# Kernel optimization log

Measured on AMD Instinct MI355X. Metric: run time of the kernel, lower is better.

## Reference

```python
import jax, jax.numpy as jnp
import numpy as np

NF, NA, NC = 100000, 400, 30   # flight, airport, carrier node counts
N = NF + NA + NC               # total nodes after type concatenation
D = 256                        # hidden_channels
B = 3                          # num_bases
R = 4                          # num_relations
E = 250000                     # edges per relation


def setup_inputs() -> dict:
    key = jax.random.key(0)
    ks = jax.random.split(key, 32)
    inp = {
        'x_flight': jax.random.normal(ks[0], (NF, 32), jnp.float32),
        'x_airport': jax.random.normal(ks[1], (NA, 16), jnp.float32),
        'x_carrier': jax.random.normal(ks[2], (NC, 8), jnp.float32),
        # per-type encoders (Linear stored as [in, out])
        'W_f': jax.random.normal(ks[3], (32, D), jnp.float32) * 0.05,
        'b_f': jnp.zeros((D,), jnp.float32),
        'W_a': jax.random.normal(ks[4], (16, D), jnp.float32) * 0.05,
        'b_a': jnp.zeros((D,), jnp.float32),
        'W_c': jax.random.normal(ks[5], (8, D), jnp.float32) * 0.05,
        'b_c': jnp.zeros((D,), jnp.float32),
        # RGCNConv layer 0: basis decomposition W_r = sum_b comp[r,b] * basis[b]
        'basis0': jax.random.normal(ks[6], (B, D, D), jnp.float32) * 0.02,
        'comp0': jax.random.normal(ks[7], (R, B), jnp.float32) * 0.5,
        'root0': jax.random.normal(ks[8], (D, D), jnp.float32) * 0.02,
        'bias0': jnp.zeros((D,), jnp.float32),
        # RGCNConv layer 1
        'basis1': jax.random.normal(ks[9], (B, D, D), jnp.float32) * 0.02,
        'comp1': jax.random.normal(ks[10], (R, B), jnp.float32) * 0.5,
        'root1': jax.random.normal(ks[11], (D, D), jnp.float32) * 0.02,
        'bias1': jnp.zeros((D,), jnp.float32),
        # readout Linear(D -> 1)
        'W_out': jax.random.normal(ks[12], (D, 1), jnp.float32) * 0.05,
        'b_out': jnp.zeros((1,), jnp.float32),
        # per-relation edge lists (local indices within src/dst node type)
        'src0': jax.random.randint(ks[13], (E,), 0, NF),
        'dst0': jax.random.randint(ks[14], (E,), 0, NA),
        'src1': jax.random.randint(ks[15], (E,), 0, NA),
        'dst1': jax.random.randint(ks[16], (E,), 0, NF),
        'src2': jax.random.randint(ks[17], (E,), 0, NF),
        'dst2': jax.random.randint(ks[18], (E,), 0, NC),
        'src3': jax.random.randint(ks[19], (E,), 0, NC),
        'dst3': jax.random.randint(ks[20], (E,), 0, NF),
    }
    return inp


def _rgcn_conv(x, basis, comp, root, bias, edges):
    """PyG RGCNConv with basis decomposition, mean aggregation per relation."""
    W = jnp.einsum('rb,bio->rio', comp, basis)  # [R, D, D]
    out = x @ root + bias                        # root/self transform
    for r, (src, dst) in enumerate(edges):       # R=4 fixed relations
        msg = x[src] @ W[r]                                        # [E, D]
        agg = jax.ops.segment_sum(msg, dst, num_segments=N)        # [N, D]
        deg = jax.ops.segment_sum(jnp.ones((dst.shape[0],), x.dtype), dst,
                                  num_segments=N)
        out = out + agg / jnp.maximum(deg, 1.0)[:, None]           # mean aggr
    return out


def reference(x_flight, x_airport, x_carrier,
              W_f, b_f, W_a, b_a, W_c, b_c,
              basis0, comp0, root0, bias0,
              basis1, comp1, root1, bias1,
              W_out, b_out,
              src0, dst0, src1, dst1, src2, dst2, src3, dst3):
    # per-type encoders + ReLU, then concat into homogeneous node tensor
    hf = jax.nn.relu(x_flight @ W_f + b_f)
    ha = jax.nn.relu(x_airport @ W_a + b_a)
    hc = jax.nn.relu(x_carrier @ W_c + b_c)
    x = jnp.concatenate([hf, ha, hc], axis=0)  # offsets: flight=0, airport=NF, carrier=NF+NA
    edges = [
        (src0, dst0 + NF),        # flight -> airport
        (src1 + NF, dst1),        # airport -> flight
        (src2, dst2 + NF + NA),   # flight -> carrier
        (src3 + NF + NA, dst3),   # carrier -> flight
    ]
    x = jax.nn.relu(_rgcn_conv(x, basis0, comp0, root0, bias0, edges))
    x = jax.nn.relu(_rgcn_conv(x, basis1, comp1, root1, bias1, edges))
    # dropout is identity in eval mode
    return (x[:NF] @ W_out + b_out).squeeze(-1)  # [NF]
```

## Files before the change

### kernel.cpp

```cpp
#include <hip/hip_runtime.h>
#include <hip/hip_bf16.h>
#include <cstdint>
#include <cstddef>

constexpr int NF = 100000;
constexpr int NA = 400;
constexpr int NC = 30;
constexpr int NN = NF + NA + NC;
constexpr int D  = 256;
constexpr int DD = D * D;
constexpr int E  = 250000;
constexpr int NSL = 128;
constexpr int FBLK = (NF + 127) / 128;

typedef __attribute__((ext_vector_type(8))) short bf16x8;
typedef __attribute__((ext_vector_type(4))) float f32x4;
typedef __attribute__((ext_vector_type(8))) ushort u16x8;

__device__ inline ushort f2bf(float f) {
    __hip_bfloat16 h = __float2bfloat16(f);
    return __builtin_bit_cast(ushort, h);
}
__device__ inline float bf2f(ushort u) {
    __hip_bfloat16 h = __builtin_bit_cast(__hip_bfloat16, u);
    return __bfloat162float(h);
}

__device__ inline void gload_lds16(const ushort* g, ushort* l) {
    __builtin_amdgcn_global_load_lds(
        (const __attribute__((address_space(1))) void*)g,
        (__attribute__((address_space(3))) void*)l, 16, 0, 0);
}

__global__ __launch_bounds__(512) void encode_mfma_kernel(
    const float* __restrict__ xf,
    const ushort* __restrict__ WtH8, const ushort* __restrict__ WtL8,
    const float* __restrict__ bfl,
    const float* __restrict__ xa, const float* __restrict__ Wa, const float* __restrict__ ba,
    const float* __restrict__ xc, const float* __restrict__ Wc, const float* __restrict__ bc,
    ushort* __restrict__ hH)
{
    const int t = threadIdx.x;
    const int b = blockIdx.x;
    if (b >= FBLK) {
        int c = t & 255;
        int i0 = t >> 8;
        int base = (b - FBLK) * 8;
        for (int i = i0; i < 8; i += 2) {
            int row = base + i;
            if (row >= NA + NC) break;
            float acc;
            if (row < NA) {
                const float* xr = xa + (size_t)row * 16;
                acc = ba[c];
                #pragma unroll
                for (int k = 0; k < 16; ++k) acc += xr[k] * Wa[k * D + c];
            } else {
                const float* xr = xc + (size_t)(row - NA) * 8;
                acc = bc[c];
                #pragma unroll
                for (int k = 0; k < 8; ++k) acc += xr[k] * Wc[k * D + c];
            }
            hH[(size_t)(NF + row) * D + c] = f2bf(fmaxf(acc, 0.f));
        }
        return;
    }
    constexpr int AOFF = 0, WHOFF = 4096, WLOFF = 12288;
    __shared__ __align__(16) ushort lds[20480];
    const int row0 = b * 128;
    const int w = t >> 6, lane = t & 63;
    const int wm = w >> 2, wn = w & 3;
    const int lr = lane & 15;
    const int lk = lane >> 4;
    {
        int r = t >> 2;
        int seg = (t & 3) * 8;
        int gr = row0 + r; if (gr >= NF) gr = NF - 1;
        const float* xr = xf + (size_t)gr * 32 + seg;
        float4 a0 = *(const float4*)xr;
        float4 a1 = *(const float4*)(xr + 4);
        u16x8 bb;
        bb[0] = f2bf(a0.x); bb[1] = f2bf(a0.y); bb[2] = f2bf(a0.z); bb[3] = f2bf(a0.w);
        bb[4] = f2bf(a1.x); bb[5] = f2bf(a1.y); bb[6] = f2bf(a1.z); bb[7] = f2bf(a1.w);
        int g = r >> 4, rr = r & 15, kg = seg >> 3;
        *(u16x8*)(lds + AOFF + g * 512 + (rr + 16 * kg) * 8) = bb;
    }
    #pragma unroll
    for (int i = 0; i < 4; ++i) {
        int u = w * 4 + i;
        int plane = u >> 4, g = u & 15;
        const ushort* src = (plane ? WtL8 : WtH8) + ((size_t)(g * 16 + lr)) * 32 + lk * 8;
        ushort* dst = lds + (plane ? WLOFF : WHOFF) + g * 512;
        gload_lds16(src, dst);
    }
    __syncthreads();
    f32x4 acc[4][4] = {};
    bf16x8 bhv[4], blv[4];
    #pragma unroll
    for (int ni = 0; ni < 4; ++ni) {
        int off = (wn * 4 + ni) * 512 + lane * 8;
        bhv[ni] = *(const bf16x8*)(lds + WHOFF + off);
        blv[ni] = *(const bf16x8*)(lds + WLOFF + off);
    }
    #pragma unroll
    for (int mi = 0; mi < 4; ++mi) {
        bf16x8 ah = *(const bf16x8*)(lds + AOFF + (wm * 4 + mi) * 512 + lane * 8);
        #pragma unroll
        for (int ni = 0; ni < 4; ++ni) {
            acc[mi][ni] = __builtin_amdgcn_mfma_f32_16x16x32_bf16(ah, bhv[ni], acc[mi][ni], 0, 0, 0);
            acc[mi][ni] = __builtin_amdgcn_mfma_f32_16x16x32_bf16(ah, blv[ni], acc[mi][ni], 0, 0, 0);
        }
    }
    constexpr int ELDW = 68;
    float* S = (float*)lds + (size_t)w * 16 * ELDW;
    const int rrow = lane >> 3;
    const int grp  = lane & 7;
    #pragma unroll
    for (int mi = 0; mi < 4; ++mi) {
        __syncthreads();
        #pragma unroll
        for (int ni = 0; ni < 4; ++ni)
            #pragma unroll
            for (int reg = 0; reg < 4; ++reg)
                S[(lk * 4 + reg) * ELDW + ni * 16 + lr] = acc[mi][ni][reg];
        __syncthreads();
        #pragma unroll
        for (int it = 0; it < 2; ++it) {
            int row_i = rrow + it * 8;
            int gr = row0 + wm * 64 + mi * 16 + row_i;
            int gc = wn * 64 + grp * 8;
            if (gr >= NF) continue;
            float4 f0 = *(const float4*)(&S[row_i * ELDW + grp * 8]);
            float4 f1 = *(const float4*)(&S[row_i * ELDW + grp * 8 + 4]);
            float4 b0 = *(const float4*)(bfl + gc);
            float4 b1 = *(const float4*)(bfl + gc + 4);
            u16x8 hh;
            hh[0] = f2bf(fmaxf(f0.x + b0.x, 0.f));
            hh[1] = f2bf(fmaxf(f0.y + b0.y, 0.f));
            hh[2] = f2bf(fmaxf(f0.z + b0.z, 0.f));
            hh[3] = f2bf(fmaxf(f0.w + b0.w, 0.f));
            hh[4] = f2bf(fmaxf(f1.x + b1.x, 0.f));
            hh[5] = f2bf(fmaxf(f1.y + b1.y, 0.f));
            hh[6] = f2bf(fmaxf(f1.z + b1.z, 0.f));
            hh[7] = f2bf(fmaxf(f1.w + b1.w, 0.f));
            *(u16x8*)(hH + (size_t)gr * D + gc) = hh;
        }
    }
}

__global__ __launch_bounds__(256) void wsplit_kernel(
    const float* __restrict__ root, ushort* __restrict__ WtH, ushort* __restrict__ WtL)
{
    int n = blockIdx.x, k = threadIdx.x;
    float w = root[(size_t)k * D + n];
    ushort hi = f2bf(w);
    WtH[(size_t)n * D + k] = hi;
    WtL[(size_t)n * D + k] = f2bf(w - bf2f(hi));
}

__global__ __launch_bounds__(256) void wr_kernel(
    const float* __restrict__ basis, const float* __restrict__ comp,
    float* __restrict__ wr)
{
    int idx = blockIdx.x * 256 + threadIdx.x;
    int r = idx >> 16;
    int io = idx & (DD - 1);
    wr[idx] = comp[r * 3 + 0] * basis[io]
            + comp[r * 3 + 1] * basis[DD + io]
            + comp[r * 3 + 2] * basis[2 * DD + io];
}

__global__ __launch_bounds__(256) void deg_count_kernel(
    const int* __restrict__ dst1, const int* __restrict__ dst3,
    int* __restrict__ deg1, int* __restrict__ deg3)
{
    int idx = blockIdx.x * 256 + threadIdx.x;
    if (idx >= 2 * E) return;
    if (idx < E) atomicAdd(&deg1[dst1[idx]], 1);
    else         atomicAdd(&deg3[dst3[idx - E]], 1);
}

__global__ __launch_bounds__(256) void hist02_kernel(
    const int* __restrict__ dst0, const int* __restrict__ dst2,
    int* __restrict__ bh0, int* __restrict__ bh2,
    int* __restrict__ deg13z, float* __restrict__ aggz,
    const float* __restrict__ Wf, ushort* __restrict__ WfTH, ushort* __restrict__ WfTL)
{
    __shared__ int hist[NA];
    int b = blockIdx.x;
    for (int i = b * 256 + threadIdx.x; i < 2 * NF; i += 2 * NSL * 256)
        deg13z[i] = 0;
    for (int i = b * 256 + threadIdx.x; i < (NA + NC) * D; i += 2 * NSL * 256)
        aggz[i] = 0.f;
    if (b < 32) {
        int n = threadIdx.x;
        float wv = Wf[(size_t)b * D + n];
        ushort hi = f2bf(wv);
        WfTH[(size_t)n * 32 + b] = hi;
        WfTL[(size_t)n * 32 + b] = f2bf(wv - bf2f(hi));
    }
    bool isR2 = (b >= NSL);
    int sl = isR2 ? b - NSL : b;
    const int* dst = isR2 ? dst2 : dst0;
    int nb = isR2 ? NC : NA;
    for (int i = threadIdx.x; i < nb; i += 256) hist[i] = 0;
    __syncthreads();
    int lo = (int)((long long)E * sl / NSL);
    int hi = (int)((long long)E * (sl + 1) / NSL);
    for (int e = lo + threadIdx.x; e < hi; e += 256)
        atomicAdd(&hist[dst[e]], 1);
    __syncthreads();
    int* bh = isR2 ? (bh2 + sl * NC) : (bh0 + sl * NA);
    for (int i = threadIdx.x; i < nb; i += 256) bh[i] = hist[i];
}

__global__ __launch_bounds__(512) void scan02_kernel(
    int* __restrict__ bh0, int* __restrict__ bh2,
    int* __restrict__ rp0, int* __restrict__ rp2,
    float* __restrict__ inv0, float* __restrict__ inv2)
{
    __shared__ int tot[512];
    __shared__ int exc[512];
    int t = threadIdx.x;
    int cnt = 0;
    if (t < NA) {
        int s = 0;
        for (int sl = 0; sl < NSL; ++sl) {
            int v = bh0[sl * NA + t]; bh0[sl * NA + t] = s; s += v;
        }
        cnt = s;
    } else if (t < NA + NC) {
        int bin = t - NA; int s = 0;
        for (int sl = 0; sl < NSL; ++sl) {
            int v = bh2[sl * NC + bin]; bh2[sl * NC + bin] = s; s += v;
        }
        cnt = s;
    }
    tot[t] = cnt;
    __syncthreads();
    for (int ofs = 1; ofs < 512; ofs <<= 1) {
        int v = (t >= ofs) ? tot[t - ofs] : 0;
        __syncthreads();
        tot[t] += v;
        __syncthreads();
    }
    int ex = tot[t] - cnt;
    if (t < NA) {
        exc[t] = ex;
        rp0[t] = ex;
        inv0[t] = 1.0f / (float)(cnt > 1 ? cnt : 1);
        if (t == 0) { rp0[NA] = E; rp2[NC] = E; }
    } else if (t < NA + NC) {
        exc[t] = ex - E;
        rp2[t - NA] = ex - E;
        inv2[t - NA] = 1.0f / (float)(cnt > 1 ? cnt : 1);
    } else exc[t] = 0;
    __syncthreads();
    for (int idx = t; idx < NSL * NA; idx += 512) {
        int sl = idx / NA; int bin = idx - sl * NA;
        bh0[idx] += exc[bin];
    }
    for (int idx = t; idx < NSL * NC; idx += 512) {
        int sl = idx / NC; int bin = idx - sl * NC;
        bh2[idx] += exc[NA + bin];
    }
}

__global__ __launch_bounds__(256) void fill02_kernel(
    const int* __restrict__ src0, const int* __restrict__ dst0,
    const int* __restrict__ src2, const int* __restrict__ dst2,
    const int* __restrict__ bh0, const int* __restrict__ bh2,
    int* __restrict__ csr0, int* __restrict__ csr2)
{
    __shared__ int cur[NA];
    int b = blockIdx.x;
    bool isR2 = (b >= NSL);
    int sl = isR2 ? b - NSL : b;
    const int* src = isR2 ? src2 : src0;
    const int* dst = isR2 ? dst2 : dst0;
    const int* bh  = isR2 ? (bh2 + sl * NC) : (bh0 + sl * NA);
    int* csr       = isR2 ? csr2 : csr0;
    int nb = isR2 ? NC : NA;
    for (int i = threadIdx.x; i < nb; i += 256) cur[i] = bh[i];
    __syncthreads();
    int lo = (int)((long long)E * sl / NSL);
    int hi = (int)((long long)E * (sl + 1) / NSL);
    for (int e = lo + threadIdx.x; e < hi; e += 256) {
        int pos = atomicAdd(&cur[dst[e]], 1);
        csr[pos] = src[e];
    }
}

__global__ __launch_bounds__(1024) void scanA_kernel(
    const int* __restrict__ deg1, const int* __restrict__ deg3, int* __restrict__ bsum)
{
    __shared__ int s[1024];
    int b = blockIdx.x;
    bool isR3 = (b >= 98);
    const int* deg = isR3 ? deg3 : deg1;
    int chunk = isR3 ? b - 98 : b;
    int i = chunk * 1024 + threadIdx.x;
    int v = (i < NF) ? deg[i] : 0;
    s[threadIdx.x] = v;
    __syncthreads();
    for (int ofs = 512; ofs > 0; ofs >>= 1) {
        if ((int)threadIdx.x < ofs) s[threadIdx.x] += s[threadIdx.x + ofs];
        __syncthreads();
    }
    if (threadIdx.x == 0) bsum[(isR3 ? 128 : 0) + chunk] = s[0];
}

__global__ __launch_bounds__(1024) void scanC_kernel(
    const int* __restrict__ deg1, const int* __restrict__ deg3,
    const int* __restrict__ bsum,
    int* __restrict__ rp1, int* __restrict__ rp3,
    int* __restrict__ cu1, int* __restrict__ cu3,
    float* __restrict__ inv1, float* __restrict__ inv3)
{
    __shared__ int s[1024];
    __shared__ int s2[256];
    int tid = threadIdx.x;
    int b = blockIdx.x;
    int vb = 0;
    if (tid < 256) {
        vb = ((tid & 127) < 98) ? bsum[tid] : 0;
        s2[tid] = vb;
    }
    __syncthreads();
    for (int ofs = 1; ofs < 128; ofs <<= 1) {
        int a = 0;
        if (tid < 256 && (tid & 127) >= ofs) a = s2[tid - ofs];
        __syncthreads();
        if (tid < 256) s2[tid] += a;
        __syncthreads();
    }
    if (tid < 256) s2[tid] -= vb;
    __syncthreads();
    const int* deg; int* rp; int* cu; float* inv; int chunk; int prefix;
    if (b < 98) { deg = deg1; rp = rp1; cu = cu1; inv = inv1; chunk = b;      prefix = s2[chunk]; }
    else        { deg = deg3; rp = rp3; cu = cu3; inv = inv3; chunk = b - 98; prefix = s2[128 + chunk]; }
    int i = chunk * 1024 + tid;
    int v = (i < NF) ? deg[i] : 0;
    s[tid] = v;
    __syncthreads();
    for (int ofs = 1; ofs < 1024; ofs <<= 1) {
        int a = (tid >= ofs) ? s[tid - ofs] : 0;
        __syncthreads();
        s[tid] += a;
        __syncthreads();
    }
    int ex = prefix + s[tid] - v;
    if (i < NF) {
        rp[i] = ex;
        cu[i] = ex;
        inv[i] = 1.0f / (float)(v > 1 ? v : 1);
    }
    if (i == 0) rp[NF] = E;
}

__global__ __launch_bounds__(256) void csr_fill13_kernel(
    const int* __restrict__ src1, const int* __restrict__ dst1,
    const int* __restrict__ src3, const int* __restrict__ dst3,
    int* __restrict__ cu1, int* __restrict__ cu3,
    int* __restrict__ csr1, int* __restrict__ csr3)
{
    int idx = blockIdx.x * 256 + threadIdx.x;
    if (idx >= 2 * E) return;
    if (idx < E) {
        int pos = atomicAdd(&cu1[dst1[idx]], 1);
        csr1[pos] = src1[idx];
    } else {
        int e = idx - E;
        int pos = atomicAdd(&cu3[dst3[e]], 1);
        csr3[pos] = src3[e];
    }
}

__global__ __launch_bounds__(256) void y_kernel(
    const ushort* __restrict__ hH, const float* __restrict__ wr,
    float* __restrict__ y)
{
    int row = blockIdx.x;
    int c = threadIdx.x;
    const ushort* sH = hH + (size_t)(NF + row) * D;
    const float* W = wr + (size_t)((row < NA) ? 1 : 3) * DD;
    float acc = 0.f;
    #pragma unroll 8
    for (int k = 0; k < D; ++k) acc += bf2f(sH[k]) * W[k * D + c];
    y[(size_t)row * D + c] = acc;
}

__global__ __launch_bounds__(512) void gemm_mfma(
    const ushort* __restrict__ A,
    const ushort* __restrict__ WtH, const ushort* __restrict__ WtL,
    const float* __restrict__ bias,
    ushort* __restrict__ G, int nrows)
{
    constexpr int BM = 128, BK = 32;
    constexpr int PLANE = BM * BK;
    constexpr int BUF = 3 * PLANE;
    constexpr int LDW = 36;
    __shared__ __align__(16) ushort lds[2 * BUF];
    const int t = threadIdx.x;
    const int row0 = blockIdx.x * BM;
    const int col0 = blockIdx.y * BM;
    const int w = t >> 6, lane = t & 63;
    const int wm = w >> 2, wn = w & 3;
    const int lr = lane & 15;
    const int lk = lane >> 4;
    f32x4 acc[4][2] = {};

    const ushort* sp[3];
    int dofs[3];
    #pragma unroll
    for (int i = 0; i < 3; ++i) {
        int idx = w * 3 + i;
        int plane = idx >> 3, g = idx & 7;
        const ushort* base = (plane == 0) ? A : (plane == 1) ? WtH : WtL;
        int r = ((plane == 0) ? row0 : col0) + g * 16 + lr;
        if (plane == 0 && r >= nrows) r = nrows - 1;
        sp[i] = base + (size_t)r * D + lk * 8;
        dofs[i] = plane * PLANE + g * 512;
    }

    auto stage = [&](int kt, int buf) {
        ushort* bb = lds + buf * BUF;
        int k0 = kt * BK;
        #pragma unroll
        for (int i = 0; i < 3; ++i)
            gload_lds16(sp[i] + k0, bb + dofs[i]);
    };
    auto compute = [&](int buf) {
        const ushort* base = lds + buf * BUF;
        const ushort* As  = base;
        const ushort* WsH = base + PLANE;
        const ushort* WsL = base + 2 * PLANE;
        bf16x8 bh[2], bl[2];
        #pragma unroll
        for (int ni = 0; ni < 2; ++ni) {
            int off = (wn * 2 + ni) * 512 + lane * 8;
            bh[ni] = *(const bf16x8*)(&WsH[off]);
            bl[ni] = *(const bf16x8*)(&WsL[off]);
        }
        #pragma unroll
        for (int mi = 0; mi < 4; ++mi) {
            int off = (wm * 4 + mi) * 512 + lane * 8;
            bf16x8 ah = *(const bf16x8*)(&As[off]);
            #pragma unroll
            for (int ni = 0; ni < 2; ++ni) {
                acc[mi][ni] = __builtin_amdgcn_mfma_f32_16x16x32_bf16(ah, bh[ni], acc[mi][ni], 0, 0, 0);
                acc[mi][ni] = __builtin_amdgcn_mfma_f32_16x16x32_bf16(ah, bl[ni], acc[mi][ni], 0, 0, 0);
            }
        }
    };

    stage(0, 0);
    stage(1, 1);
#define PIPE_ITER(KT, PEND)                                        \
    asm volatile("s_waitcnt vmcnt(" #PEND ")" ::: "memory");       \
    __builtin_amdgcn_s_barrier();                                  \
    __builtin_amdgcn_sched_barrier(0);                             \
    compute((KT) & 1);                                             \
    __builtin_amdgcn_s_barrier();                                  \
    __builtin_amdgcn_sched_barrier(0);                             \
    if ((KT) + 2 < 8) stage((KT) + 2, (KT) & 1);
    PIPE_ITER(0, 3)
    PIPE_ITER(1, 3)
    PIPE_ITER(2, 3)
    PIPE_ITER(3, 3)
    PIPE_ITER(4, 3)
    PIPE_ITER(5, 3)
    PIPE_ITER(6, 3)
    PIPE_ITER(7, 0)
#undef PIPE_ITER

    __syncthreads();
    float* S = (float*)lds + (size_t)w * 16 * LDW;
    const int rrow = lane >> 2;
    const int grp  = lane & 3;
    #pragma unroll
    for (int mi = 0; mi < 4; ++mi) {
        __syncthreads();
        #pragma unroll
        for (int ni = 0; ni < 2; ++ni)
            #pragma unroll
            for (int reg = 0; reg < 4; ++reg)
                S[(lk * 4 + reg) * LDW + ni * 16 + lr] = acc[mi][ni][reg];
        __syncthreads();
        int gr = row0 + wm * 64 + mi * 16 + rrow;
        int gc = col0 + wn * 32 + grp * 8;
        if (gr >= nrows) continue;
        float4 f0 = *(const float4*)(&S[rrow * LDW + grp * 8]);
        float4 f1 = *(const float4*)(&S[rrow * LDW + grp * 8 + 4]);
        float4 b0 = *(const float4*)(bias + gc);
        float4 b1 = *(const float4*)(bias + gc + 4);
        float v[8] = {f0.x + b0.x, f0.y + b0.y, f0.z + b0.z, f0.w + b0.w,
                      f1.x + b1.x, f1.y + b1.y, f1.z + b1.z, f1.w + b1.w};
        u16x8 hh;
        #pragma unroll
        for (int j = 0; j < 8; ++j) hh[j] = f2bf(v[j]);
        *(u16x8*)(G + (size_t)gr * D + gc) = hh;
    }
}

__global__ __launch_bounds__(256) void msg_relu_kernel(
    ushort* __restrict__ G,
    const float* __restrict__ y,
    const int* __restrict__ rp1, const int* __restrict__ csr1, const float* __restrict__ inv1,
    const int* __restrict__ rp3, const int* __restrict__ csr3, const float* __restrict__ inv3)
{
    int wid = (blockIdx.x * 256 + threadIdx.x) >> 6;
    int lane = threadIdx.x & 63;
    int row = wid * 2 + (lane >> 5);
    if (row >= NF) return;
    int c = (lane & 31) * 8;
    size_t o = (size_t)row * D + c;
    u16x8 gh = *(const u16x8*)(G + o);
    float v[8];
    #pragma unroll
    for (int j = 0; j < 8; ++j) v[j] = bf2f(gh[j]);
    float m[8] = {};
    int e0 = rp1[row], e1 = rp1[row + 1];
    for (int e = e0; e < e1; ++e) {
        const float* yr = y + (size_t)csr1[e] * D + c;
        float4 u0 = *(const float4*)yr;
        float4 u1 = *(const float4*)(yr + 4);
        m[0] += u0.x; m[1] += u0.y; m[2] += u0.z; m[3] += u0.w;
        m[4] += u1.x; m[5] += u1.y; m[6] += u1.z; m[7] += u1.w;
    }
    float s1 = inv1[row];
    #pragma unroll
    for (int j = 0; j < 8; ++j) { v[j] += s1 * m[j]; m[j] = 0.f; }
    e0 = rp3[row]; e1 = rp3[row + 1];
    for (int e = e0; e < e1; ++e) {
        const float* yr = y + (size_t)(NA + csr3[e]) * D + c;
        float4 u0 = *(const float4*)yr;
        float4 u1 = *(const float4*)(yr + 4);
        m[0] += u0.x; m[1] += u0.y; m[2] += u0.z; m[3] += u0.w;
        m[4] += u1.x; m[5] += u1.y; m[6] += u1.z; m[7] += u1.w;
    }
    float s3 = inv3[row];
    u16x8 oh;
    #pragma unroll
    for (int j = 0; j < 8; ++j) oh[j] = f2bf(fmaxf(v[j] + s3 * m[j], 0.f));
    *(u16x8*)(G + o) = oh;
}

__global__ __launch_bounds__(256) void msg_readout_kernel(
    const ushort* __restrict__ G,
    const float* __restrict__ y,
    const int* __restrict__ rp1, const int* __restrict__ csr1, const float* __restrict__ inv1,
    const int* __restrict__ rp3, const int* __restrict__ csr3, const float* __restrict__ inv3,
    const float* __restrict__ wout, const float* __restrict__ bout,
    float* __restrict__ out)
{
    int wid = (blockIdx.x * 256 + threadIdx.x) >> 6;
    int lane = threadIdx.x & 63;
    int row = wid * 2 + (lane >> 5);
    if (row >= NF) return;
    int c = (lane & 31) * 8;
    size_t o = (size_t)row * D + c;
    u16x8 gh = *(const u16x8*)(G + o);
    float v[8];
    #pragma unroll
    for (int j = 0; j < 8; ++j) v[j] = bf2f(gh[j]);
    float m[8] = {};
    int e0 = rp1[row], e1 = rp1[row + 1];
    for (int e = e0; e < e1; ++e) {
        const float* yr = y + (size_t)csr1[e] * D + c;
        float4 u0 = *(const float4*)yr;
        float4 u1 = *(const float4*)(yr + 4);
        m[0] += u0.x; m[1] += u0.y; m[2] += u0.z; m[3] += u0.w;
        m[4] += u1.x; m[5] += u1.y; m[6] += u1.z; m[7] += u1.w;
    }
    float s1 = inv1[row];
    #pragma unroll
    for (int j = 0; j < 8; ++j) { v[j] += s1 * m[j]; m[j] = 0.f; }
    e0 = rp3[row]; e1 = rp3[row + 1];
    for (int e = e0; e < e1; ++e) {
        const float* yr = y + (size_t)(NA + csr3[e]) * D + c;
        float4 u0 = *(const float4*)yr;
        float4 u1 = *(const float4*)(yr + 4);
        m[0] += u0.x; m[1] += u0.y; m[2] += u0.z; m[3] += u0.w;
        m[4] += u1.x; m[5] += u1.y; m[6] += u1.z; m[7] += u1.w;
    }
    float s3 = inv3[row];
    float4 w0 = *(const float4*)(wout + c);
    float4 w1 = *(const float4*)(wout + c + 4);
    float wv[8] = {w0.x, w0.y, w0.z, w0.w, w1.x, w1.y, w1.z, w1.w};
    float pr = 0.f;
    #pragma unroll
    for (int j = 0; j < 8; ++j) pr += fmaxf(v[j] + s3 * m[j], 0.f) * wv[j];
    pr += __shfl_xor(pr, 1);
    pr += __shfl_xor(pr, 2);
    pr += __shfl_xor(pr, 4);
    pr += __shfl_xor(pr, 8);
    pr += __shfl_xor(pr, 16);
    if ((lane & 31) == 0) out[row] = pr + bout[0];
}

__global__ __launch_bounds__(256) void agg_small_kernel(
    const ushort* __restrict__ hH,
    const int* __restrict__ rp0, const int* __restrict__ csr0,
    const int* __restrict__ rp2, const int* __restrict__ csr2,
    float* __restrict__ agg)
{
    __shared__ float red[4][256];
    int b = blockIdx.x;
    const int* rp; const int* csr; int dstn, chunk, nch; float* arow;
    if (b < NA * 4) { dstn = b >> 2; chunk = b & 3; nch = 4;  rp = rp0; csr = csr0; arow = agg + (size_t)dstn * D; }
    else { int bb = b - NA * 4; dstn = bb >> 6; chunk = bb & 63; nch = 64; rp = rp2; csr = csr2; arow = agg + (size_t)(NA + dstn) * D; }
    int s = rp[dstn], e = rp[dstn + 1];
    int cnt = e - s;
    int lo = s + (int)((long long)cnt * chunk / nch);
    int hi = s + (int)((long long)cnt * (chunk + 1) / nch);
    int w = threadIdx.x >> 6, lane = threadIdx.x & 63;
    int span = hi - lo;
    int wlo = lo + (int)((long long)span * w / 4);
    int whi = lo + (int)((long long)span * (w + 1) / 4);
    int half = lane >> 5;
    int ch8 = (lane & 31) * 8;
    float acc[8] = {};
    int p = wlo;
    for (; p + 1 < whi; p += 2) {
        int r = csr[p + half];
        u16x8 v = *(const u16x8*)(hH + (size_t)r * D + ch8);
        #pragma unroll
        for (int j = 0; j < 8; ++j) acc[j] += bf2f(v[j]);
    }
    if (p < whi && half == 0) {
        int r = csr[p];
        u16x8 v = *(const u16x8*)(hH + (size_t)r * D + ch8);
        #pragma unroll
        for (int j = 0; j < 8; ++j) acc[j] += bf2f(v[j]);
    }
    #pragma unroll
    for (int j = 0; j < 8; ++j) acc[j] += __shfl_xor(acc[j], 32);
    if (lane < 32) {
        #pragma unroll
        for (int j = 0; j < 8; ++j) red[w][ch8 + j] = acc[j];
    }
    __syncthreads();
    int c = threadIdx.x;
    float total = red[0][c] + red[1][c] + red[2][c] + red[3][c];
    atomicAdd(arow + c, total);
}

__global__ __launch_bounds__(256) void smallT_kernel(
    const float* __restrict__ agg, const float* __restrict__ wr,
    const float* __restrict__ inv0, const float* __restrict__ inv2,
    ushort* __restrict__ G)
{
    int row = blockIdx.x;
    int c = threadIdx.x;
    const float* a = agg + (size_t)row * D;
    const float* W = wr + (size_t)((row < NA) ? 0 : 2) * DD;
    float scale = (row < NA) ? inv0[row] : inv2[row - NA];
    float acc = 0.f;
    #pragma unroll 8
    for (int k = 0; k < D; ++k) acc += a[k] * W[k * D + c];
    size_t o = (size_t)(NF + row) * D + c;
    G[o] = f2bf(fmaxf(bf2f(G[o]) + scale * acc, 0.f));
}

extern "C" void kernel_launch(void* const* d_in, const int* in_sizes, int n_in,
                              void* d_out, int out_size, void* d_ws, size_t ws_size,
                              hipStream_t stream)
{
    const float* xf = (const float*)d_in[0];
    const float* xa = (const float*)d_in[1];
    const float* xc = (const float*)d_in[2];
    const float* Wf = (const float*)d_in[3];
    const float* bf = (const float*)d_in[4];
    const float* Wa = (const float*)d_in[5];
    const float* ba = (const float*)d_in[6];
    const float* Wc = (const float*)d_in[7];
    const float* bc = (const float*)d_in[8];
    const float* basis0 = (const float*)d_in[9];
    const float* comp0  = (const float*)d_in[10];
    const float* root0  = (const float*)d_in[11];
    const float* bias0  = (const float*)d_in[12];
    const float* basis1 = (const float*)d_in[13];
    const float* comp1  = (const float*)d_in[14];
    const float* root1  = (const float*)d_in[15];
    const float* bias1  = (const float*)d_in[16];
    const float* Wout = (const float*)d_in[17];
    const float* bout = (const float*)d_in[18];
    const int* src0 = (const int*)d_in[19];
    const int* dst0 = (const int*)d_in[20];
    const int* src1 = (const int*)d_in[21];
    const int* dst1 = (const int*)d_in[22];
    const int* src2 = (const int*)d_in[23];
    const int* dst2 = (const int*)d_in[24];
    const int* src3 = (const int*)d_in[25];
    const int* dst3 = (const int*)d_in[26];
    float* out = (float*)d_out;

    char* ws = (char*)d_ws;
    size_t off = 0;
    auto alloc = [&](size_t bytes) -> char* {
        char* p = ws + off;
        off = (off + bytes + 255) & ~(size_t)255;
        return p;
    };
    ushort* hH  = (ushort*)alloc((size_t)NN * D * 2);
    ushort* gH  = (ushort*)alloc((size_t)NN * D * 2);
    ushort* g2H = hH;
    ushort* WtH = (ushort*)alloc((size_t)DD * 2);
    ushort* WtL = (ushort*)alloc((size_t)DD * 2);
    ushort* WfTH = (ushort*)alloc((size_t)D * 32 * 2);
    ushort* WfTL = (ushort*)alloc((size_t)D * 32 * 2);
    float* wrbuf  = (float*)alloc((size_t)4 * DD * 4);
    float* ybuf   = (float*)alloc((size_t)(NA + NC) * D * 4);
    float* aggbuf = (float*)alloc((size_t)(NA + NC) * D * 4);
    int*   deg13  = (int*)  alloc((size_t)2 * NF * 4);
    int* deg1 = deg13; int* deg3 = deg13 + NF;
    float* inv1 = (float*)alloc((size_t)NF * 4);
    float* inv3 = (float*)alloc((size_t)NF * 4);
    float* inv0 = (float*)alloc((size_t)NA * 4);
    float* inv2 = (float*)alloc((size_t)NC * 4);
    int* rp0 = (int*)alloc((NA + 1) * 4);
    int* rp1 = (int*)alloc((size_t)(NF + 1) * 4);
    int* rp2 = (int*)alloc((NC + 1) * 4);
    int* rp3 = (int*)alloc((size_t)(NF + 1) * 4);
    int* cu1 = (int*)alloc((size_t)(NF + 1) * 4);
    int* cu3 = (int*)alloc((size_t)(NF + 1) * 4);
    int* csr0 = (int*)alloc((size_t)E * 4);
    int* csr1 = (int*)alloc((size_t)E * 4);
    int* csr2 = (int*)alloc((size_t)E * 4);
    int* csr3 = (int*)alloc((size_t)E * 4);
    int* bsum = (int*)alloc(256 * 4);
    int* bh0  = (int*)alloc((size_t)NSL * NA * 4);
    int* bh2  = (int*)alloc((size_t)NSL * NC * 4);
    (void)ws_size; (void)in_sizes; (void)n_in; (void)out_size;

    hist02_kernel<<<2 * NSL, 256, 0, stream>>>(dst0, dst2, bh0, bh2, deg13, aggbuf,
                                               Wf, WfTH, WfTL);
    scan02_kernel<<<1, 512, 0, stream>>>(bh0, bh2, rp0, rp2, inv0, inv2);
    fill02_kernel<<<2 * NSL, 256, 0, stream>>>(src0, dst0, src2, dst2, bh0, bh2, csr0, csr2);

    deg_count_kernel<<<(2 * E + 255) / 256, 256, 0, stream>>>(dst1, dst3, deg1, deg3);
    scanA_kernel<<<196, 1024, 0, stream>>>(deg1, deg3, bsum);
    scanC_kernel<<<196, 1024, 0, stream>>>(deg1, deg3, bsum, rp1, rp3, cu1, cu3, inv1, inv3);
    csr_fill13_kernel<<<(2 * E + 255) / 256, 256, 0, stream>>>(
        src1, dst1, src3, dst3, cu1, cu3, csr1, csr3);

    encode_mfma_kernel<<<FBLK + (NA + NC + 7) / 8, 512, 0, stream>>>(
        xf, WfTH, WfTL, bf, xa, Wa, ba, xc, Wc, bc, hH);

    wsplit_kernel<<<D, D, 0, stream>>>(root0, WtH, WtL);
    wr_kernel<<<4 * DD / 256, 256, 0, stream>>>(basis0, comp0, wrbuf);
    y_kernel<<<NA + NC, 256, 0, stream>>>(hH, wrbuf, ybuf);
    gemm_mfma<<<dim3((NN + 127) / 128, 2), 512, 0, stream>>>(
        hH, WtH, WtL, bias0, gH, NN);
    agg_small_kernel<<<NA * 4 + NC * 64, 256, 0, stream>>>(
        hH, rp0, csr0, rp2, csr2, aggbuf);
    smallT_kernel<<<NA + NC, 256, 0, stream>>>(aggbuf, wrbuf, inv0, inv2, gH);
    msg_relu_kernel<<<(NF / 2 * 64 + 255) / 256, 256, 0, stream>>>(
        gH, ybuf, rp1, csr1, inv1, rp3, csr3, inv3);

    wsplit_kernel<<<D, D, 0, stream>>>(root1, WtH, WtL);
    wr_kernel<<<4 * DD / 256, 256, 0, stream>>>(basis1, comp1, wrbuf);
    y_kernel<<<NA + NC, 256, 0, stream>>>(gH, wrbuf, ybuf);
    gemm_mfma<<<dim3((NF + 127) / 128, 2), 512, 0, stream>>>(
        gH, WtH, WtL, bias1, g2H, NF);
    msg_readout_kernel<<<(NF / 2 * 64 + 255) / 256, 256, 0, stream>>>(
        g2H, ybuf, rp1, csr1, inv1, rp3, csr3, inv3, Wout, bout, out);
}
```

Baseline: 368.0 us.

## Merge preprocessing kernels into fewer launches with block-range dispatch

Independent preprocessing stages (histograms, degree counts, root weight split, basis combination for both layers) are merged into one kernel that dispatches on block index. Scan stages are paired the same way, and the CSR fill for relations 1/3 now runs inside the encoder launch. This cuts the launch count and serialization bubbles between many small kernels. In exchange it needs separate weight buffers per layer, and the degree zeroing moves to a memset.

```diff
diff --git a/kernel.cpp b/kernel.cpp
--- a/kernel.cpp
+++ b/kernel.cpp
@@ -12,6 +12,15 @@
 constexpr int E  = 250000;
 constexpr int NSL = 128;
 constexpr int FBLK = (NF + 127) / 128;
+constexpr int TAILB = (NA + NC + 7) / 8;
+constexpr int F13B = (2 * E + 511) / 512;
+
+constexpr int K1_HIST_END = 2 * NSL;
+constexpr int K1_DEG_END  = K1_HIST_END + (2 * E + 255) / 256;
+constexpr int K1_WS0_END  = K1_DEG_END + 256;
+constexpr int K1_WS1_END  = K1_WS0_END + 256;
+constexpr int K1_WR0_END  = K1_WS1_END + 1024;
+constexpr int K1_WR1_END  = K1_WR0_END + 1024;
 
 typedef __attribute__((ext_vector_type(8))) short bf16x8;
 typedef __attribute__((ext_vector_type(4))) float f32x4;
@@ -32,16 +41,251 @@
         (__attribute__((address_space(3))) void*)l, 16, 0, 0);
 }
 
-__global__ __launch_bounds__(512) void encode_mfma_kernel(
+__global__ __launch_bounds__(256) void prep_kernel(
+    const int* __restrict__ dst0, const int* __restrict__ dst2,
+    int* __restrict__ bh0, int* __restrict__ bh2,
+    float* __restrict__ aggz,
+    const float* __restrict__ Wf, ushort* __restrict__ WfTH, ushort* __restrict__ WfTL,
+    const int* __restrict__ dst1, const int* __restrict__ dst3,
+    int* __restrict__ deg1, int* __restrict__ deg3,
+    const float* __restrict__ root0, ushort* __restrict__ WtH0, ushort* __restrict__ WtL0,
+    const float* __restrict__ root1, ushort* __restrict__ WtH1, ushort* __restrict__ WtL1,
+    const float* __restrict__ basis0, const float* __restrict__ comp0, float* __restrict__ wr0,
+    const float* __restrict__ basis1, const float* __restrict__ comp1, float* __restrict__ wr1)
+{
+    __shared__ int hist[NA];
+    const int b = blockIdx.x;
+    const int t = threadIdx.x;
+    if (b < K1_HIST_END) {
+        for (int i = b * 256 + t; i < (NA + NC) * D; i += K1_HIST_END * 256)
+            aggz[i] = 0.f;
+        if (b < 32) {
+            float wv = Wf[(size_t)b * D + t];
+            ushort hi = f2bf(wv);
+            WfTH[(size_t)t * 32 + b] = hi;
+            WfTL[(size_t)t * 32 + b] = f2bf(wv - bf2f(hi));
+        }
+        bool isR2 = (b >= NSL);
+        int sl = isR2 ? b - NSL : b;
+        const int* dst = isR2 ? dst2 : dst0;
+        int nb = isR2 ? NC : NA;
+        for (int i = t; i < nb; i += 256) hist[i] = 0;
+        __syncthreads();
+        int lo = (int)((long long)E * sl / NSL);
+        int hi = (int)((long long)E * (sl + 1) / NSL);
+        for (int e = lo + t; e < hi; e += 256)
+            atomicAdd(&hist[dst[e]], 1);
+        __syncthreads();
+        int* bh = isR2 ? (bh2 + sl * NC) : (bh0 + sl * NA);
+        for (int i = t; i < nb; i += 256) bh[i] = hist[i];
+    } else if (b < K1_DEG_END) {
+        int idx = (b - K1_HIST_END) * 256 + t;
+        if (idx < 2 * E) {
+            if (idx < E) atomicAdd(&deg1[dst1[idx]], 1);
+            else         atomicAdd(&deg3[dst3[idx - E]], 1);
+        }
+    } else if (b < K1_WS0_END) {
+        int n = b - K1_DEG_END;
+        float w = root0[(size_t)t * D + n];
+        ushort hi = f2bf(w);
+        WtH0[(size_t)n * D + t] = hi;
+        WtL0[(size_t)n * D + t] = f2bf(w - bf2f(hi));
+    } else if (b < K1_WS1_END) {
+        int n = b - K1_WS0_END;
+        float w = root1[(size_t)t * D + n];
+        ushort hi = f2bf(w);
+        WtH1[(size_t)n * D + t] = hi;
+        WtL1[(size_t)n * D + t] = f2bf(w - bf2f(hi));
+    } else if (b < K1_WR0_END) {
+        int idx = (b - K1_WS1_END) * 256 + t;
+        int r = idx >> 16;
+        int io = idx & (DD - 1);
+        wr0[idx] = comp0[r * 3 + 0] * basis0[io]
+                 + comp0[r * 3 + 1] * basis0[DD + io]
+                 + comp0[r * 3 + 2] * basis0[2 * DD + io];
+    } else {
+        int idx = (b - K1_WR0_END) * 256 + t;
+        int r = idx >> 16;
+        int io = idx & (DD - 1);
+        wr1[idx] = comp1[r * 3 + 0] * basis1[io]
+                 + comp1[r * 3 + 1] * basis1[DD + io]
+                 + comp1[r * 3 + 2] * basis1[2 * DD + io];
+    }
+}
+
+__global__ __launch_bounds__(1024) void scan_kernel(
+    const int* __restrict__ deg1, const int* __restrict__ deg3,
+    int* __restrict__ bsum,
+    int* __restrict__ bh0, int* __restrict__ bh2,
+    int* __restrict__ rp0, int* __restrict__ rp2,
+    float* __restrict__ inv0, float* __restrict__ inv2)
+{
+    __shared__ int s[1024];
+    __shared__ int tot[512];
+    __shared__ int exc[512];
+    const int b = blockIdx.x;
+    const int t = threadIdx.x;
+    if (b < 196) {
+        bool isR3 = (b >= 98);
+        const int* deg = isR3 ? deg3 : deg1;
+        int chunk = isR3 ? b - 98 : b;
+        int i = chunk * 1024 + t;
+        int v = (i < NF) ? deg[i] : 0;
+        s[t] = v;
+        __syncthreads();
+        for (int ofs = 512; ofs > 0; ofs >>= 1) {
+            if (t < ofs) s[t] += s[t + ofs];
+            __syncthreads();
+        }
+        if (t == 0) bsum[(isR3 ? 128 : 0) + chunk] = s[0];
+        return;
+    }
+    int cnt = 0;
+    if (t < NA) {
+        int ss = 0;
+        for (int sl = 0; sl < NSL; ++sl) {
+            int v = bh0[sl * NA + t]; bh0[sl * NA + t] = ss; ss += v;
+        }
+        cnt = ss;
+    } else if (t < NA + NC) {
+        int bin = t - NA; int ss = 0;
+        for (int sl = 0; sl < NSL; ++sl) {
+            int v = bh2[sl * NC + bin]; bh2[sl * NC + bin] = ss; ss += v;
+        }
+        cnt = ss;
+    }
+    if (t < 512) tot[t] = cnt;
+    __syncthreads();
+    for (int ofs = 1; ofs < 512; ofs <<= 1) {
+        int v = 0;
+        if (t < 512 && t >= ofs) v = tot[t - ofs];
+        __syncthreads();
+        if (t < 512) tot[t] += v;
+        __syncthreads();
+    }
+    if (t < 512) {
+        int ex = tot[t] - cnt;
+        if (t < NA) {
+            exc[t] = ex;
+            rp0[t] = ex;
+            inv0[t] = 1.0f / (float)(cnt > 1 ? cnt : 1);
+            if (t == 0) { rp0[NA] = E; rp2[NC] = E; }
+        } else if (t < NA + NC) {
+            exc[t] = ex - E;
+            rp2[t - NA] = ex - E;
+            inv2[t - NA] = 1.0f / (float)(cnt > 1 ? cnt : 1);
+        } else exc[t] = 0;
+    }
+    __syncthreads();
+    for (int idx = t; idx < NSL * NA; idx += 1024) {
+        int sl = idx / NA; int bin = idx - sl * NA;
+        bh0[idx] += exc[bin];
+    }
+    for (int idx = t; idx < NSL * NC; idx += 1024) {
+        int sl = idx / NC; int bin = idx - sl * NC;
+        bh2[idx] += exc[NA + bin];
+    }
+}
+
+__global__ __launch_bounds__(1024) void fill_scan_kernel(
+    const int* __restrict__ src0, const int* __restrict__ dst0,
+    const int* __restrict__ src2, const int* __restrict__ dst2,
+    const int* __restrict__ bh0, const int* __restrict__ bh2,
+    int* __restrict__ csr0, int* __restrict__ csr2,
+    const int* __restrict__ deg1, const int* __restrict__ deg3,
+    const int* __restrict__ bsum,
+    int* __restrict__ rp1, int* __restrict__ rp3,
+    int* __restrict__ cu1, int* __restrict__ cu3,
+    float* __restrict__ inv1, float* __restrict__ inv3)
+{
+    __shared__ int s[1024];
+    __shared__ int s2[256];
+    const int b = blockIdx.x;
+    const int t = threadIdx.x;
+    if (b < 2 * NSL) {
+        bool isR2 = (b >= NSL);
+        int sl = isR2 ? b - NSL : b;
+        const int* src = isR2 ? src2 : src0;
+        const int* dst = isR2 ? dst2 : dst0;
+        const int* bh  = isR2 ? (bh2 + sl * NC) : (bh0 + sl * NA);
+        int* csr       = isR2 ? csr2 : csr0;
+        int nb = isR2 ? NC : NA;
+        for (int i = t; i < nb; i += 1024) s[i] = bh[i];
+        __syncthreads();
+        int lo = (int)((long long)E * sl / NSL);
+        int hi = (int)((long long)E * (sl + 1) / NSL);
+        for (int e = lo + t; e < hi; e += 1024) {
+            int pos = atomicAdd(&s[dst[e]], 1);
+            csr[pos] = src[e];
+        }
+        return;
+    }
+    const int bb = b - 2 * NSL;
+    int vb = 0;
+    if (t < 256) {
+        vb = ((t & 127) < 98) ? bsum[t] : 0;
+        s2[t] = vb;
+    }
+    __syncthreads();
+    for (int ofs = 1; ofs < 128; ofs <<= 1) {
+        int a = 0;
+        if (t < 256 && (t & 127) >= ofs) a = s2[t - ofs];
+        __syncthreads();
+        if (t < 256) s2[t] += a;
+        __syncthreads();
+    }
+    if (t < 256) s2[t] -= vb;
+    __syncthreads();
+    const int* deg; int* rp; int* cu; float* inv; int chunk; int prefix;
+    if (bb < 98) { deg = deg1; rp = rp1; cu = cu1; inv = inv1; chunk = bb;      prefix = s2[chunk]; }
+    else         { deg = deg3; rp = rp3; cu = cu3; inv = inv3; chunk = bb - 98; prefix = s2[128 + chunk]; }
+    int i = chunk * 1024 + t;
+    int v = (i < NF) ? deg[i] : 0;
+    s[t] = v;
+    __syncthreads();
+    for (int ofs = 1; ofs < 1024; ofs <<= 1) {
+        int a = (t >= ofs) ? s[t - ofs] : 0;
+        __syncthreads();
+        s[t] += a;
+        __syncthreads();
+    }
+    int ex = prefix + s[t] - v;
+    if (i < NF) {
+        rp[i] = ex;
+        cu[i] = ex;
+        inv[i] = 1.0f / (float)(v > 1 ? v : 1);
+    }
+    if (i == 0) rp[NF] = E;
+}
+
+__global__ __launch_bounds__(512) void encode_fill_kernel(
     const float* __restrict__ xf,
     const ushort* __restrict__ WtH8, const ushort* __restrict__ WtL8,
     const float* __restrict__ bfl,
     const float* __restrict__ xa, const float* __restrict__ Wa, const float* __restrict__ ba,
     const float* __restrict__ xc, const float* __restrict__ Wc, const float* __restrict__ bc,
-    ushort* __restrict__ hH)
+    ushort* __restrict__ hH,
+    const int* __restrict__ src1, const int* __restrict__ dst1,
+    const int* __restrict__ src3, const int* __restrict__ dst3,
+    int* __restrict__ cu1, int* __restrict__ cu3,
+    int* __restrict__ csr1, int* __restrict__ csr3)
 {
     const int t = threadIdx.x;
     const int b = blockIdx.x;
+    if (b >= FBLK + TAILB) {
+        int idx = (b - FBLK - TAILB) * 512 + t;
+        if (idx < 2 * E) {
+            if (idx < E) {
+                int pos = atomicAdd(&cu1[dst1[idx]], 1);
+                csr1[pos] = src1[idx];
+            } else {
+                int e = idx - E;
+                int pos = atomicAdd(&cu3[dst3[e]], 1);
+                csr3[pos] = src3[e];
+            }
+        }
+        return;
+    }
     if (b >= FBLK) {
         int c = t & 255;
         int i0 = t >> 8;
@@ -145,234 +389,6 @@
             hh[7] = f2bf(fmaxf(f1.w + b1.w, 0.f));
             *(u16x8*)(hH + (size_t)gr * D + gc) = hh;
         }
-    }
-}
-
-__global__ __launch_bounds__(256) void wsplit_kernel(
-    const float* __restrict__ root, ushort* __restrict__ WtH, ushort* __restrict__ WtL)
-{
-    int n = blockIdx.x, k = threadIdx.x;
-    float w = root[(size_t)k * D + n];
-    ushort hi = f2bf(w);
-    WtH[(size_t)n * D + k] = hi;
-    WtL[(size_t)n * D + k] = f2bf(w - bf2f(hi));
-}
-
-__global__ __launch_bounds__(256) void wr_kernel(
-    const float* __restrict__ basis, const float* __restrict__ comp,
-    float* __restrict__ wr)
-{
-    int idx = blockIdx.x * 256 + threadIdx.x;
-    int r = idx >> 16;
-    int io = idx & (DD - 1);
-    wr[idx] = comp[r * 3 + 0] * basis[io]
-            + comp[r * 3 + 1] * basis[DD + io]
-            + comp[r * 3 + 2] * basis[2 * DD + io];
-}
-
-__global__ __launch_bounds__(256) void deg_count_kernel(
-    const int* __restrict__ dst1, const int* __restrict__ dst3,
-    int* __restrict__ deg1, int* __restrict__ deg3)
-{
-    int idx = blockIdx.x * 256 + threadIdx.x;
-    if (idx >= 2 * E) return;
-    if (idx < E) atomicAdd(&deg1[dst1[idx]], 1);
-    else         atomicAdd(&deg3[dst3[idx - E]], 1);
-}
-
-__global__ __launch_bounds__(256) void hist02_kernel(
-    const int* __restrict__ dst0, const int* __restrict__ dst2,
-    int* __restrict__ bh0, int* __restrict__ bh2,
-    int* __restrict__ deg13z, float* __restrict__ aggz,
-    const float* __restrict__ Wf, ushort* __restrict__ WfTH, ushort* __restrict__ WfTL)
-{
-    __shared__ int hist[NA];
-    int b = blockIdx.x;
-    for (int i = b * 256 + threadIdx.x; i < 2 * NF; i += 2 * NSL * 256)
-        deg13z[i] = 0;
-    for (int i = b * 256 + threadIdx.x; i < (NA + NC) * D; i += 2 * NSL * 256)
-        aggz[i] = 0.f;
-    if (b < 32) {
-        int n = threadIdx.x;
-        float wv = Wf[(size_t)b * D + n];
-        ushort hi = f2bf(wv);
-        WfTH[(size_t)n * 32 + b] = hi;
-        WfTL[(size_t)n * 32 + b] = f2bf(wv - bf2f(hi));
-    }
-    bool isR2 = (b >= NSL);
-    int sl = isR2 ? b - NSL : b;
-    const int* dst = isR2 ? dst2 : dst0;
-    int nb = isR2 ? NC : NA;
-    for (int i = threadIdx.x; i < nb; i += 256) hist[i] = 0;
-    __syncthreads();
-    int lo = (int)((long long)E * sl / NSL);
-    int hi = (int)((long long)E * (sl + 1) / NSL);
-    for (int e = lo + threadIdx.x; e < hi; e += 256)
-        atomicAdd(&hist[dst[e]], 1);
-    __syncthreads();
-    int* bh = isR2 ? (bh2 + sl * NC) : (bh0 + sl * NA);
-    for (int i = threadIdx.x; i < nb; i += 256) bh[i] = hist[i];
-}
-
-__global__ __launch_bounds__(512) void scan02_kernel(
-    int* __restrict__ bh0, int* __restrict__ bh2,
-    int* __restrict__ rp0, int* __restrict__ rp2,
-    float* __restrict__ inv0, float* __restrict__ inv2)
-{
-    __shared__ int tot[512];
-    __shared__ int exc[512];
-    int t = threadIdx.x;
-    int cnt = 0;
-    if (t < NA) {
-        int s = 0;
-        for (int sl = 0; sl < NSL; ++sl) {
-            int v = bh0[sl * NA + t]; bh0[sl * NA + t] = s; s += v;
-        }
-        cnt = s;
-    } else if (t < NA + NC) {
-        int bin = t - NA; int s = 0;
-        for (int sl = 0; sl < NSL; ++sl) {
-            int v = bh2[sl * NC + bin]; bh2[sl * NC + bin] = s; s += v;
-        }
-        cnt = s;
-    }
-    tot[t] = cnt;
-    __syncthreads();
-    for (int ofs = 1; ofs < 512; ofs <<= 1) {
-        int v = (t >= ofs) ? tot[t - ofs] : 0;
-        __syncthreads();
-        tot[t] += v;
-        __syncthreads();
-    }
-    int ex = tot[t] - cnt;
-    if (t < NA) {
-        exc[t] = ex;
-        rp0[t] = ex;
-        inv0[t] = 1.0f / (float)(cnt > 1 ? cnt : 1);
-        if (t == 0) { rp0[NA] = E; rp2[NC] = E; }
-    } else if (t < NA + NC) {
-        exc[t] = ex - E;
-        rp2[t - NA] = ex - E;
-        inv2[t - NA] = 1.0f / (float)(cnt > 1 ? cnt : 1);
-    } else exc[t] = 0;
-    __syncthreads();
-    for (int idx = t; idx < NSL * NA; idx += 512) {
-        int sl = idx / NA; int bin = idx - sl * NA;
-        bh0[idx] += exc[bin];
-    }
-    for (int idx = t; idx < NSL * NC; idx += 512) {
-        int sl = idx / NC; int bin = idx - sl * NC;
-        bh2[idx] += exc[NA + bin];
-    }
-}
-
-__global__ __launch_bounds__(256) void fill02_kernel(
-    const int* __restrict__ src0, const int* __restrict__ dst0,
-    const int* __restrict__ src2, const int* __restrict__ dst2,
-    const int* __restrict__ bh0, const int* __restrict__ bh2,
-    int* __restrict__ csr0, int* __restrict__ csr2)
-{
-    __shared__ int cur[NA];
-    int b = blockIdx.x;
-    bool isR2 = (b >= NSL);
-    int sl = isR2 ? b - NSL : b;
-    const int* src = isR2 ? src2 : src0;
-    const int* dst = isR2 ? dst2 : dst0;
-    const int* bh  = isR2 ? (bh2 + sl * NC) : (bh0 + sl * NA);
-    int* csr       = isR2 ? csr2 : csr0;
-    int nb = isR2 ? NC : NA;
-    for (int i = threadIdx.x; i < nb; i += 256) cur[i] = bh[i];
-    __syncthreads();
-    int lo = (int)((long long)E * sl / NSL);
-    int hi = (int)((long long)E * (sl + 1) / NSL);
-    for (int e = lo + threadIdx.x; e < hi; e += 256) {
-        int pos = atomicAdd(&cur[dst[e]], 1);
-        csr[pos] = src[e];
-    }
-}
-
-__global__ __launch_bounds__(1024) void scanA_kernel(
-    const int* __restrict__ deg1, const int* __restrict__ deg3, int* __restrict__ bsum)
-{
-    __shared__ int s[1024];
-    int b = blockIdx.x;
-    bool isR3 = (b >= 98);
-    const int* deg = isR3 ? deg3 : deg1;
-    int chunk = isR3 ? b - 98 : b;
-    int i = chunk * 1024 + threadIdx.x;
-    int v = (i < NF) ? deg[i] : 0;
-    s[threadIdx.x] = v;
-    __syncthreads();
-    for (int ofs = 512; ofs > 0; ofs >>= 1) {
-        if ((int)threadIdx.x < ofs) s[threadIdx.x] += s[threadIdx.x + ofs];
-        __syncthreads();
-    }
-    if (threadIdx.x == 0) bsum[(isR3 ? 128 : 0) + chunk] = s[0];
-}
-
-__global__ __launch_bounds__(1024) void scanC_kernel(
-    const int* __restrict__ deg1, const int* __restrict__ deg3,
-    const int* __restrict__ bsum,
-    int* __restrict__ rp1, int* __restrict__ rp3,
-    int* __restrict__ cu1, int* __restrict__ cu3,
-    float* __restrict__ inv1, float* __restrict__ inv3)
-{
-    __shared__ int s[1024];
-    __shared__ int s2[256];
-    int tid = threadIdx.x;
-    int b = blockIdx.x;
-    int vb = 0;
-    if (tid < 256) {
-        vb = ((tid & 127) < 98) ? bsum[tid] : 0;
-        s2[tid] = vb;
-    }
-    __syncthreads();
-    for (int ofs = 1; ofs < 128; ofs <<= 1) {
-        int a = 0;
-        if (tid < 256 && (tid & 127) >= ofs) a = s2[tid - ofs];
-        __syncthreads();
-        if (tid < 256) s2[tid] += a;
-        __syncthreads();
-    }
-    if (tid < 256) s2[tid] -= vb;
-    __syncthreads();
-    const int* deg; int* rp; int* cu; float* inv; int chunk; int prefix;
-    if (b < 98) { deg = deg1; rp = rp1; cu = cu1; inv = inv1; chunk = b;      prefix = s2[chunk]; }
-    else        { deg = deg3; rp = rp3; cu = cu3; inv = inv3; chunk = b - 98; prefix = s2[128 + chunk]; }
-    int i = chunk * 1024 + tid;
-    int v = (i < NF) ? deg[i] : 0;
-    s[tid] = v;
-    __syncthreads();
-    for (int ofs = 1; ofs < 1024; ofs <<= 1) {
-        int a = (tid >= ofs) ? s[tid - ofs] : 0;
-        __syncthreads();
-        s[tid] += a;
-        __syncthreads();
-    }
-    int ex = prefix + s[tid] - v;
-    if (i < NF) {
-        rp[i] = ex;
-        cu[i] = ex;
-        inv[i] = 1.0f / (float)(v > 1 ? v : 1);
-    }
-    if (i == 0) rp[NF] = E;
-}
-
-__global__ __launch_bounds__(256) void csr_fill13_kernel(
-    const int* __restrict__ src1, const int* __restrict__ dst1,
-    const int* __restrict__ src3, const int* __restrict__ dst3,
-    int* __restrict__ cu1, int* __restrict__ cu3,
-    int* __restrict__ csr1, int* __restrict__ csr3)
-{
-    int idx = blockIdx.x * 256 + threadIdx.x;
-    if (idx >= 2 * E) return;
-    if (idx < E) {
-        int pos = atomicAdd(&cu1[dst1[idx]], 1);
-        csr1[pos] = src1[idx];
-    } else {
-        int e = idx - E;
-        int pos = atomicAdd(&cu3[dst3[e]], 1);
-        csr3[pos] = src3[e];
     }
 }
 
@@ -706,11 +722,14 @@
     ushort* hH  = (ushort*)alloc((size_t)NN * D * 2);
     ushort* gH  = (ushort*)alloc((size_t)NN * D * 2);
     ushort* g2H = hH;
-    ushort* WtH = (ushort*)alloc((size_t)DD * 2);
-    ushort* WtL = (ushort*)alloc((size_t)DD * 2);
+    ushort* WtH0 = (ushort*)alloc((size_t)DD * 2);
+    ushort* WtL0 = (ushort*)alloc((size_t)DD * 2);
+    ushort* WtH1 = (ushort*)alloc((size_t)DD * 2);
+    ushort* WtL1 = (ushort*)alloc((size_t)DD * 2);
     ushort* WfTH = (ushort*)alloc((size_t)D * 32 * 2);
     ushort* WfTL = (ushort*)alloc((size_t)D * 32 * 2);
-    float* wrbuf  = (float*)alloc((size_t)4 * DD * 4);
+    float* wr0    = (float*)alloc((size_t)4 * DD * 4);
+    float* wr1    = (float*)alloc((size_t)4 * DD * 4);
     float* ybuf   = (float*)alloc((size_t)(NA + NC) * D * 4);
     float* aggbuf = (float*)alloc((size_t)(NA + NC) * D * 4);
     int*   deg13  = (int*)  alloc((size_t)2 * NF * 4);
@@ -734,36 +753,37 @@
     int* bh2  = (int*)alloc((size_t)NSL * NC * 4);
     (void)ws_size; (void)in_sizes; (void)n_in; (void)out_size;
 
-    hist02_kernel<<<2 * NSL, 256, 0, stream>>>(dst0, dst2, bh0, bh2, deg13, aggbuf,
-                                               Wf, WfTH, WfTL);
-    scan02_kernel<<<1, 512, 0, stream>>>(bh0, bh2, rp0, rp2, inv0, inv2);
-    fill02_kernel<<<2 * NSL, 256, 0, stream>>>(src0, dst0, src2, dst2, bh0, bh2, csr0, csr2);
-
-    deg_count_kernel<<<(2 * E + 255) / 256, 256, 0, stream>>>(dst1, dst3, deg1, deg3);
-    scanA_kernel<<<196, 1024, 0, stream>>>(deg1, deg3, bsum);
-    scanC_kernel<<<196, 1024, 0, stream>>>(deg1, deg3, bsum, rp1, rp3, cu1, cu3, inv1, inv3);
-    csr_fill13_kernel<<<(2 * E + 255) / 256, 256, 0, stream>>>(
+    hipMemsetAsync(deg13, 0, (size_t)2 * NF * 4, stream);
+
+    prep_kernel<<<K1_WR1_END, 256, 0, stream>>>(
+        dst0, dst2, bh0, bh2, aggbuf, Wf, WfTH, WfTL,
+        dst1, dst3, deg1, deg3,
+        root0, WtH0, WtL0, root1, WtH1, WtL1,
+        basis0, comp0, wr0, basis1, comp1, wr1);
+
+    scan_kernel<<<197, 1024, 0, stream>>>(
+        deg1, deg3, bsum, bh0, bh2, rp0, rp2, inv0, inv2);
+
+    fill_scan_kernel<<<2 * NSL + 196, 1024, 0, stream>>>(
+        src0, dst0, src2, dst2, bh0, bh2, csr0, csr2,
+        deg1, deg3, bsum, rp1, rp3, cu1, cu3, inv1, inv3);
+
+    encode_fill_kernel<<<FBLK + TAILB + F13B, 512, 0, stream>>>(
+        xf, WfTH, WfTL, bf, xa, Wa, ba, xc, Wc, bc, hH,
         src1, dst1, src3, dst3, cu1, cu3, csr1, csr3);
 
-    encode_mfma_kernel<<<FBLK + (NA + NC + 7) / 8, 512, 0, stream>>>(
-        xf, WfTH, WfTL, bf, xa, Wa, ba, xc, Wc, bc, hH);
-
-    wsplit_kernel<<<D, D, 0, stream>>>(root0, WtH, WtL);
-    wr_kernel<<<4 * DD / 256, 256, 0, stream>>>(basis0, comp0, wrbuf);
-    y_kernel<<<NA + NC, 256, 0, stream>>>(hH, wrbuf, ybuf);
+    y_kernel<<<NA + NC, 256, 0, stream>>>(hH, wr0, ybuf);
     gemm_mfma<<<dim3((NN + 127) / 128, 2), 512, 0, stream>>>(
-        hH, WtH, WtL, bias0, gH, NN);
+        hH, WtH0, WtL0, bias0, gH, NN);
     agg_small_kernel<<<NA * 4 + NC * 64, 256, 0, stream>>>(
         hH, rp0, csr0, rp2, csr2, aggbuf);
-    smallT_kernel<<<NA + NC, 256, 0, stream>>>(aggbuf, wrbuf, inv0, inv2, gH);
+    smallT_kernel<<<NA + NC, 256, 0, stream>>>(aggbuf, wr0, inv0, inv2, gH);
     msg_relu_kernel<<<(NF / 2 * 64 + 255) / 256, 256, 0, stream>>>(
         gH, ybuf, rp1, csr1, inv1, rp3, csr3, inv3);
 
-    wsplit_kernel<<<D, D, 0, stream>>>(root1, WtH, WtL);
-    wr_kernel<<<4 * DD / 256, 256, 0, stream>>>(basis1, comp1, wrbuf);
-    y_kernel<<<NA + NC, 256, 0, stream>>>(gH, wrbuf, ybuf);
+    y_kernel<<<NA + NC, 256, 0, stream>>>(gH, wr1, ybuf);
     gemm_mfma<<<dim3((NF + 127) / 128, 2), 512, 0, stream>>>(
-        gH, WtH, WtL, bias1, g2H, NF);
+        gH, WtH1, WtL1, bias1, g2H, NF);
     msg_readout_kernel<<<(NF / 2 * 64 + 255) / 256, 256, 0, stream>>>(
         g2H, ybuf, rp1, csr1, inv1, rp3, csr3, inv3, Wout, bout, out);
 }
```

New measurement: 351.4 us. 4.5% less time.
